# Kernel tuning notes

Hardware: AMD Instinct MI355X
Metric: run time of the kernel (lower is better)

The kernel has to match this reference:

```python
import jax, jax.numpy as jnp
import numpy as np

HEADS = 8


def _gat(X, A, Wq, Wk, Wv, Wo, units):
    B, N, _ = X.shape
    # QKV projections -> [B, H, N, units]
    Q = (X @ Wq).reshape(B, N, HEADS, units).transpose(0, 2, 1, 3)
    K = (X @ Wk).reshape(B, N, HEADS, units).transpose(0, 2, 1, 3)
    V = (X @ Wv).reshape(B, N, HEADS, units).transpose(0, 2, 1, 3)
    scores = jnp.einsum('bhnd,bhmd->bhnm', Q, K) / jnp.sqrt(jnp.float32(units))
    # source adds A * -1e9 (masks where A == 1)
    scores = scores + A[:, None, :, :] * (-1e9)
    w = jax.nn.softmax(scores, axis=-1)  # dropout off at inference
    ctx = jnp.einsum('bhnm,bhmd->bhnd', w, V)
    ctx = ctx.transpose(0, 2, 1, 3).reshape(B, N, HEADS * units)
    return ctx @ Wo


def setup_inputs() -> dict:
    key = jax.random.key(0)
    ks = jax.random.split(key, 16)
    B, N, F = 8, 1024, 64
    u1, u2 = 128, 64
    g = lambda k, s: (jax.random.normal(k, s, dtype=jnp.float32)
                      * np.sqrt(2.0 / (s[0] + s[-1])).astype(np.float32))
    X = jax.random.normal(ks[0], (B, N, F), dtype=jnp.float32)
    A = jax.random.bernoulli(ks[1], 0.5, (B, N, N)).astype(jnp.float32)
    return {
        'X': X, 'A': A,
        'Wq1': g(ks[2], (F, u1 * HEADS)), 'Wk1': g(ks[3], (F, u1 * HEADS)),
        'Wv1': g(ks[4], (F, u1 * HEADS)), 'Wo1': g(ks[5], (u1 * HEADS, u1)),
        'Wq2': g(ks[6], (u1, u2 * HEADS)), 'Wk2': g(ks[7], (u1, u2 * HEADS)),
        'Wv2': g(ks[8], (u1, u2 * HEADS)), 'Wo2': g(ks[9], (u2 * HEADS, u2)),
        'W1': g(ks[10], (u2, 32)), 'b1': jnp.zeros((32,), jnp.float32),
        'W2': g(ks[11], (32, 16)), 'b2': jnp.zeros((16,), jnp.float32),
        'W3': g(ks[12], (16, 1)), 'b3': jnp.zeros((1,), jnp.float32),
    }


def reference(X, A, Wq1, Wk1, Wv1, Wo1, Wq2, Wk2, Wv2, Wo2,
              W1, b1, W2, b2, W3, b3):
    h = _gat(X, A, Wq1, Wk1, Wv1, Wo1, 128)   # [B, N, 128]
    h = _gat(h, A, Wq2, Wk2, Wv2, Wo2, 64)    # [B, N, 64]
    h = jnp.mean(h, axis=1)                   # [B, 64]
    h = jax.nn.relu(h @ W1 + b1)
    h = jax.nn.relu(h @ W2 + b2)
    return h @ W3 + b3                        # [B, 1]
```

## Files before the change

### kernel.cpp

```cpp
#include <hip/hip_runtime.h>
#include <hip/hip_bf16.h>
#include <math.h>

#define NB 8
#define NN 1024
#define NH 8

typedef __attribute__((ext_vector_type(8))) short bf16x8;
typedef __attribute__((ext_vector_type(4))) float f32x4;
typedef unsigned int u32;
typedef unsigned short u16;

__device__ __forceinline__ u16 f2bf(float f) {
    union { float f; u32 u; } v; v.f = f;
    const u32 u = v.u;
    return (u16)((u + 0x7fffu + ((u >> 16) & 1u)) >> 16);
}

__device__ __forceinline__ u32 cvt_pk_bf16(float lo, float hi) {
    u32 r;
    asm("v_cvt_pk_bf16_f32 %0, %1, %2" : "=v"(r) : "v"(lo), "v"(hi));
    return r;
}

__global__ __launch_bounds__(256) void mask_bits(const float* __restrict__ A,
                                                 u32* __restrict__ bits) {
    const int row = blockIdx.x;
    const int tid = threadIdx.x;
    const int lane = tid & 63;
    const float* __restrict__ ar = A + (size_t)row * NN;
#pragma unroll
    for (int it = 0; it < 4; ++it) {
        const int i = it * 256 + tid;
        const unsigned long long bal = __ballot(ar[i] != 0.0f);
        const int w0 = (it * 256 + (tid & ~63)) >> 5;
        if (lane == 0)  bits[(size_t)row * 32 + w0]     = (u32)bal;
        if (lane == 32) bits[(size_t)row * 32 + w0 + 1] = (u32)(bal >> 32);
    }
}

__global__ __launch_bounds__(256)
void cvt_bf16(const float* __restrict__ in, u16* __restrict__ out) {
    const int i = blockIdx.x * 256 + threadIdx.x;
    const float4 a = ((const float4*)in)[2 * i];
    const float4 b = ((const float4*)in)[2 * i + 1];
    u16 t[8] = {f2bf(a.x), f2bf(a.y), f2bf(a.z), f2bf(a.w),
                f2bf(b.x), f2bf(b.y), f2bf(b.z), f2bf(b.w)};
    ((uint4*)out)[i] = *(uint4*)t;
}

template <int KIN, int HD>
__global__ __launch_bounds__(256)
void cvt_qkvT(const float* __restrict__ Wq, const float* __restrict__ Wk,
              const float* __restrict__ Wv, u16* __restrict__ WT) {
    const int idx = blockIdx.x * 256 + threadIdx.x;
    const int c  = idx / (KIN / 8);
    const int f0 = (idx % (KIN / 8)) * 8;
    const float* __restrict__ W = (c < HD) ? Wq : (c < 2 * HD) ? Wk : Wv;
    const int cc = c % HD;
    u16 tmp[8];
#pragma unroll
    for (int j = 0; j < 8; ++j)
        tmp[j] = f2bf(W[(size_t)(f0 + j) * HD + cc]);
    *(uint4*)&WT[(size_t)c * KIN + f0] = *(uint4*)tmp;
}

template <int CIN, int COUT>
__global__ __launch_bounds__(256)
void cvt_woT(const float* __restrict__ Wo, u16* __restrict__ WoT) {
    const int idx = blockIdx.x * 256 + threadIdx.x;
    const int n  = idx / (CIN / 8);
    const int k0 = (idx % (CIN / 8)) * 8;
    u16 tmp[8];
#pragma unroll
    for (int j = 0; j < 8; ++j)
        tmp[j] = f2bf(Wo[(size_t)(k0 + j) * COUT + n]);
    *(uint4*)&WoT[(size_t)n * CIN + k0] = *(uint4*)tmp;
}

template <int KIN, int HD, int D>
__global__ __launch_bounds__(256)
void proj_mfma(const u16* __restrict__ Xb,
               const u16* __restrict__ WT,
               u16* __restrict__ Qb,
               u16* __restrict__ Kb,
               u16* __restrict__ VT,
               const float qscale) {
    constexpr int NKT = KIN / 32;
    constexpr int NTW = (3 * HD / 16) / 4;

    const int tid  = threadIdx.x;
    const int w    = tid >> 6;
    const int lane = tid & 63;
    const int g    = lane >> 4;
    const int q16  = lane & 15;
    const int r0   = blockIdx.x * 16;
    const int b    = r0 >> 10;
    const int n0   = r0 & 1023;
    const int ch   = n0 >> 5;
    const int grp  = (n0 >> 4) & 1;

    bf16x8 af[NKT];
#pragma unroll
    for (int t = 0; t < NKT; ++t)
        af[t] = *(const bf16x8*)&Xb[(size_t)(r0 + q16) * KIN + t * 32 + g * 8];

#pragma unroll 1
    for (int i = 0; i < NTW; ++i) {
        const int nt = w + 4 * i;
        const int c0 = nt * 16;
        f32x4 acc = (f32x4)0.f;
#pragma unroll
        for (int t = 0; t < NKT; ++t) {
            const bf16x8 wf = *(const bf16x8*)&WT[(size_t)(c0 + q16) * KIN + t * 32 + g * 8];
            acc = __builtin_amdgcn_mfma_f32_16x16x32_bf16(af[t], wf, acc, 0, 0, 0);
        }

        const int wcl = c0 / HD;
        const int cc  = c0 % HD;
        const int h   = cc / D;
        const int d0  = cc % D;
        const int bh  = b * NH + h;

        if (wcl == 2) {
            u16 tmp[4];
#pragma unroll
            for (int r = 0; r < 4; ++r) tmp[r] = f2bf(acc[r]);
            *(uint2*)&VT[(((size_t)bh * 32 + ch) * D + d0 + q16) * 32
                         + 8 * g + 4 * grp] = *(uint2*)tmp;
        } else {
            u16* __restrict__ O = wcl ? Kb : Qb;
            const float sc = wcl ? 1.0f : qscale;
#pragma unroll
            for (int r = 0; r < 4; ++r)
                O[((size_t)bh * NN + n0 + 4 * g + r) * D + d0 + q16] = f2bf(acc[r] * sc);
        }
    }
}

template <int D>
__global__ __launch_bounds__(256, 2)
void attn_v12(const u16* __restrict__ Qb,
              const u16* __restrict__ Kb,
              const u16* __restrict__ VT,
              const u32* __restrict__ bits,
              u16* __restrict__ Ob) {
    constexpr int ND4 = D / 32;
    constexpr int NDT = D / 16;
    constexpr int KROWB = 2 * D;
    constexpr int KBYTES = 64 * KROWB;
    constexpr int KU = (D == 128) ? 4 : 2;

    const int tid  = threadIdx.x;
    const int w    = tid >> 6;
    const int lane = tid & 63;
    const int g    = lane >> 4;
    const int q16  = lane & 15;

    const int xcd    = blockIdx.x & 7;
    const int within = blockIdx.x >> 3;
    const int bh     = xcd * 8 + (within >> 3);
    const int b      = bh >> 3, h = bh & 7;
    const int q0     = ((within & 7) * 4 + w) * 32;

    const u16* __restrict__ qbase = Qb + (size_t)bh * NN * D;
    const u16* __restrict__ kbase = Kb + (size_t)bh * NN * D;
    const u16* __restrict__ vbase = VT + (size_t)bh * 32 * D * 32;
    const u32* __restrict__ brow0 = bits + ((size_t)b * NN + q0 + q16) * 32;
    const u32* __restrict__ brow1 = brow0 + 16 * 32;

    __shared__ alignas(16) char KsB[2][KBYTES];

    const int kRow = tid >> 2;
    const int kU0  = (tid & 3) * KU;

    bf16x8 qf[2][ND4];
#pragma unroll
    for (int qs = 0; qs < 2; ++qs)
#pragma unroll
        for (int f = 0; f < ND4; ++f)
            qf[qs][f] = *(const bf16x8*)
                &qbase[(size_t)(q0 + qs * 16 + q16) * D + f * 32 + g * 8];

    f32x4 acc[2][NDT];
    f32x4 accL[2];
#pragma unroll
    for (int qs = 0; qs < 2; ++qs) {
        accL[qs] = (f32x4)0.f;
#pragma unroll
        for (int dt = 0; dt < NDT; ++dt) acc[qs][dt] = (f32x4)0.f;
    }

    const short oneb = (short)0x3F80;
    const bf16x8 ones = {oneb, oneb, oneb, oneb, oneb, oneb, oneb, oneb};

    uint4 skr[KU];
    auto stage_load = [&](int ch) {
        const u16* src = kbase + (size_t)(ch * 64 + kRow) * D + kU0 * 8;
#pragma unroll
        for (int i = 0; i < KU; ++i) skr[i] = *(const uint4*)(src + i * 8);
    };
    auto stage_write = [&](int buf) {
        char* kr = KsB[buf] + kRow * KROWB;
#pragma unroll
        for (int i = 0; i < KU; ++i)
            *(uint4*)(kr + (((kU0 + i) ^ (kRow & 7)) * 16)) = skr[i];
    };

    stage_load(0);
    stage_write(0);
    stage_load(1);
    __syncthreads();

#pragma unroll 1
    for (int ch = 0; ch < 16; ++ch) {
        const int cur = ch & 1;
        if (ch + 1 < 16) stage_write(cur ^ 1);
        if (ch + 2 < 16) stage_load(ch + 2);

        bf16x8 vf[2][NDT];
#pragma unroll
        for (int kg = 0; kg < 2; ++kg)
#pragma unroll
            for (int dt = 0; dt < NDT; ++dt)
                vf[kg][dt] = *(const bf16x8*)
                    &vbase[((size_t)(ch * 2 + kg) * D + dt * 16 + q16) * 32 + 8 * g];

        const uint2 bwA = *(const uint2*)(brow0 + ch * 2);
        const uint2 bwB = *(const uint2*)(brow1 + ch * 2);

        f32x4 s[2][4];
#pragma unroll
        for (int qs = 0; qs < 2; ++qs)
#pragma unroll
            for (int kb = 0; kb < 4; ++kb) s[qs][kb] = (f32x4)0.f;

        __builtin_amdgcn_s_setprio(1);
#pragma unroll
        for (int kb = 0; kb < 4; ++kb) {
            bf16x8 kf[ND4];
#pragma unroll
            for (int f = 0; f < ND4; ++f)
                kf[f] = *(const bf16x8*)
                    (KsB[cur] + (kb * 16 + q16) * KROWB + (((f * 4 + g) ^ (q16 & 7)) * 16));
#pragma unroll
            for (int f = 0; f < ND4; ++f) {
                s[0][kb] = __builtin_amdgcn_mfma_f32_16x16x32_bf16(kf[f], qf[0][f], s[0][kb], 0, 0, 0);
                s[1][kb] = __builtin_amdgcn_mfma_f32_16x16x32_bf16(kf[f], qf[1][f], s[1][kb], 0, 0, 0);
            }
        }
        __builtin_amdgcn_s_setprio(0);

        union { u32 u[4]; bf16x8 v; } pa[2][2];
#pragma unroll
        for (int qs = 0; qs < 2; ++qs) {
            const u32 w0 = qs ? bwB.x : bwA.x;
            const u32 w1 = qs ? bwB.y : bwA.y;
#pragma unroll
            for (int kb = 0; kb < 4; ++kb) {
                const u32 sh = ((kb >> 1) ? w1 : w0) >> (g * 4 + (kb & 1) * 16);
                float p[4];
#pragma unroll
                for (int r = 0; r < 4; ++r) {
                    const float e = exp2f(s[qs][kb][r]);
                    p[r] = ((sh >> r) & 1u) ? 0.f : e;
                }
                pa[qs][kb >> 1].u[(kb & 1) * 2 + 0] = cvt_pk_bf16(p[0], p[1]);
                pa[qs][kb >> 1].u[(kb & 1) * 2 + 1] = cvt_pk_bf16(p[2], p[3]);
            }
        }

        __builtin_amdgcn_s_setprio(1);
#pragma unroll
        for (int kg = 0; kg < 2; ++kg) {
            accL[0] = __builtin_amdgcn_mfma_f32_16x16x32_bf16(pa[0][kg].v, ones, accL[0], 0, 0, 0);
            accL[1] = __builtin_amdgcn_mfma_f32_16x16x32_bf16(pa[1][kg].v, ones, accL[1], 0, 0, 0);
#pragma unroll
            for (int dt = 0; dt < NDT; ++dt) {
                acc[0][dt] = __builtin_amdgcn_mfma_f32_16x16x32_bf16(pa[0][kg].v, vf[kg][dt], acc[0][dt], 0, 0, 0);
                acc[1][dt] = __builtin_amdgcn_mfma_f32_16x16x32_bf16(pa[1][kg].v, vf[kg][dt], acc[1][dt], 0, 0, 0);
            }
        }
        __builtin_amdgcn_s_setprio(0);

        __syncthreads();
    }

#pragma unroll
    for (int qs = 0; qs < 2; ++qs) {
        float ivr[4];
#pragma unroll
        for (int r = 0; r < 4; ++r) ivr[r] = 1.0f / accL[qs][r];
#pragma unroll
        for (int dt = 0; dt < NDT; ++dt)
#pragma unroll
            for (int r = 0; r < 4; ++r) {
                const int q = q0 + qs * 16 + g * 4 + r;
                Ob[(((size_t)b * NN + q) * NH + h) * D + dt * 16 + q16] =
                    f2bf(acc[qs][dt][r] * ivr[r]);
            }
    }
}

template <int CIN, int COUT, bool BF16OUT>
__global__ __launch_bounds__(256)
void wo_mfma(const u16* __restrict__ ctxb,
             const u16* __restrict__ WoT,
             void* __restrict__ Hout) {
    constexpr int NTW = COUT / 64;
    const int tid  = threadIdx.x;
    const int w    = tid >> 6;
    const int lane = tid & 63;
    const int g    = lane >> 4;
    const int q16  = lane & 15;
    const int r0   = blockIdx.x * 16;

    f32x4 acc[NTW];
#pragma unroll
    for (int nt = 0; nt < NTW; ++nt) acc[nt] = (f32x4)0.f;

    const u16* __restrict__ arow = ctxb + (size_t)(r0 + q16) * CIN + g * 8;

#pragma unroll 4
    for (int k0 = 0; k0 < CIN; k0 += 32) {
        const bf16x8 af = *(const bf16x8*)(arow + k0);
#pragma unroll
        for (int nt = 0; nt < NTW; ++nt) {
            const int n = (w * NTW + nt) * 16 + q16;
            const bf16x8 wf = *(const bf16x8*)&WoT[(size_t)n * CIN + k0 + g * 8];
            acc[nt] = __builtin_amdgcn_mfma_f32_16x16x32_bf16(af, wf, acc[nt], 0, 0, 0);
        }
    }

#pragma unroll
    for (int nt = 0; nt < NTW; ++nt)
#pragma unroll
        for (int r = 0; r < 4; ++r) {
            const size_t off = (size_t)(r0 + 4 * g + r) * COUT + (w * NTW + nt) * 16 + q16;
            if constexpr (BF16OUT) ((u16*)Hout)[off] = f2bf(acc[nt][r]);
            else                   ((float*)Hout)[off] = acc[nt][r];
        }
}

__global__ __launch_bounds__(256)
void pool_partial(const float* __restrict__ H2, float* __restrict__ partial) {
    const int b  = blockIdx.x >> 5;
    const int ch = blockIdx.x & 31;
    const int tid = threadIdx.x;
    const int o = tid & 63;
    const int g = tid >> 6;

    __shared__ float red[4][64];
    float acc = 0.f;
#pragma unroll
    for (int i = 0; i < 8; ++i) {
        const int n = ch * 32 + g * 8 + i;
        acc += H2[((size_t)b * NN + n) * 64 + o];
    }
    red[g][o] = acc;
    __syncthreads();
    if (g == 0)
        partial[((size_t)b * 32 + ch) * 64 + o] =
            (red[0][o] + red[1][o]) + (red[2][o] + red[3][o]);
}

__global__ __launch_bounds__(256)
void pool_mlp2(const float* __restrict__ partial,
               const float* __restrict__ W1, const float* __restrict__ b1,
               const float* __restrict__ W2, const float* __restrict__ b2,
               const float* __restrict__ W3, const float* __restrict__ b3,
               float* __restrict__ out) {
    const int b = blockIdx.x;
    const int tid = threadIdx.x;
    const int o = tid & 63;
    const int g = tid >> 6;
    __shared__ float red[4][64];
    __shared__ float mean[64];
    __shared__ float h1[32];
    __shared__ float h2[16];

    float acc = 0.f;
#pragma unroll
    for (int c = 0; c < 8; ++c)
        acc += partial[((size_t)b * 32 + g * 8 + c) * 64 + o];
    red[g][o] = acc;
    __syncthreads();
    if (g == 0)
        mean[o] = ((red[0][o] + red[1][o]) + (red[2][o] + red[3][o])) * (1.0f / 1024.0f);
    __syncthreads();

    if (tid < 32) {
        float a = b1[tid];
#pragma unroll
        for (int f = 0; f < 64; ++f) a = fmaf(mean[f], W1[f * 32 + tid], a);
        h1[tid] = fmaxf(a, 0.f);
    }
    __syncthreads();
    if (tid < 16) {
        float a = b2[tid];
#pragma unroll
        for (int f = 0; f < 32; ++f) a = fmaf(h1[f], W2[f * 16 + tid], a);
        h2[tid] = fmaxf(a, 0.f);
    }
    __syncthreads();
    if (tid == 0) {
        float a = b3[0];
#pragma unroll
        for (int f = 0; f < 16; ++f) a = fmaf(h2[f], W3[f], a);
        out[b] = a;
    }
}

extern "C" void kernel_launch(void* const* d_in, const int* in_sizes, int n_in,
                              void* d_out, int out_size, void* d_ws, size_t ws_size,
                              hipStream_t stream) {
    const float* X   = (const float*)d_in[0];
    const float* A   = (const float*)d_in[1];
    const float* Wq1 = (const float*)d_in[2];
    const float* Wk1 = (const float*)d_in[3];
    const float* Wv1 = (const float*)d_in[4];
    const float* Wo1 = (const float*)d_in[5];
    const float* Wq2 = (const float*)d_in[6];
    const float* Wk2 = (const float*)d_in[7];
    const float* Wv2 = (const float*)d_in[8];
    const float* Wo2 = (const float*)d_in[9];
    const float* W1  = (const float*)d_in[10];
    const float* b1  = (const float*)d_in[11];
    const float* W2  = (const float*)d_in[12];
    const float* b2  = (const float*)d_in[13];
    const float* W3  = (const float*)d_in[14];
    const float* b3  = (const float*)d_in[15];
    float* out = (float*)d_out;

    u32* bits   = (u32*)d_ws;
    u16* base   = (u16*)(bits + 262144);
    u16* Qb1    = base;  base += 8388608;
    u16* Kb1    = base;  base += 8388608;
    u16* VT1    = base;  base += 8388608;
    u16* ctx1b  = base;  base += 8388608;
    u16* WoT1   = base;  base += 131072;
    u16* Qb2    = base;  base += 4194304;
    u16* Kb2    = base;  base += 4194304;
    u16* VT2    = base;  base += 4194304;
    u16* ctx2b  = base;  base += 4194304;
    u16* WoT2   = base;  base += 32768;
    u16* Xb     = base;  base += 524288;
    u16* WqkvT1 = base;  base += 196608;
    u16* WqkvT2 = base;  base += 196608;
    u16* H1b    = base;  base += 1048576;
    float* H2   = (float*)base;
    float* partial = H2 + 524288;

    const int ROWS = NB * NN;
    const float LOG2E = 1.4426950408889634f;

    mask_bits<<<ROWS, 256, 0, stream>>>(A, bits);
    cvt_bf16<<<ROWS * 64 / 8 / 256, 256, 0, stream>>>(X, Xb);
    cvt_qkvT<64, 1024><<<3072 * 64 / 8 / 256, 256, 0, stream>>>(Wq1, Wk1, Wv1, WqkvT1);
    cvt_qkvT<128, 512><<<1536 * 128 / 8 / 256, 256, 0, stream>>>(Wq2, Wk2, Wv2, WqkvT2);
    cvt_woT<1024, 128><<<128 * 1024 / 8 / 256, 256, 0, stream>>>(Wo1, WoT1);
    cvt_woT<512, 64><<<64 * 512 / 8 / 256, 256, 0, stream>>>(Wo2, WoT2);

    proj_mfma<64, 1024, 128><<<ROWS / 16, 256, 0, stream>>>(
        Xb, WqkvT1, Qb1, Kb1, VT1, 0.08838834764831845f * LOG2E);
    attn_v12<128><<<512, 256, 0, stream>>>(Qb1, Kb1, VT1, bits, ctx1b);
    wo_mfma<1024, 128, true><<<ROWS / 16, 256, 0, stream>>>(ctx1b, WoT1, H1b);

    proj_mfma<128, 512, 64><<<ROWS / 16, 256, 0, stream>>>(
        H1b, WqkvT2, Qb2, Kb2, VT2, 0.125f * LOG2E);
    attn_v12<64><<<512, 256, 0, stream>>>(Qb2, Kb2, VT2, bits, ctx2b);
    wo_mfma<512, 64, false><<<ROWS / 16, 256, 0, stream>>>(ctx2b, WoT2, H2);

    pool_partial<<<256, 256, 0, stream>>>(H2, partial);
    pool_mlp2<<<NB, 256, 0, stream>>>(partial, W1, b1, W2, b2, W3, b3, out);
}
```

Before: 252.0 us.

## Stage V tiles through double-buffered LDS and parametrize KV block size

The attention kernel now loads V chunks cooperatively into a padded, double-buffered shared-memory tile alongside K. Previously every wave read V fragments directly from global memory, so the four waves of a block each fetched the same data. The KV chunk size becomes a template parameter, 64 for the first layer and 128 for the second, which halves the loop trips and barriers in layer two. The cost is more LDS per block, which may affect occupancy at 2 blocks per CU, plus extra LDS traffic and register pressure.

Result: slower. 269.0 us (+6.7%).

```diff
diff --git a/kernel.cpp b/kernel.cpp
--- a/kernel.cpp
+++ b/kernel.cpp
@@ -138,18 +138,24 @@
     }
 }
 
-template <int D>
+template <int D, int KVBLK>
 __global__ __launch_bounds__(256, 2)
-void attn_v12(const u16* __restrict__ Qb,
+void attn_v13(const u16* __restrict__ Qb,
               const u16* __restrict__ Kb,
               const u16* __restrict__ VT,
               const u32* __restrict__ bits,
               u16* __restrict__ Ob) {
     constexpr int ND4 = D / 32;
     constexpr int NDT = D / 16;
+    constexpr int NCH = NN / KVBLK;
+    constexpr int NKB = KVBLK / 16;
+    constexpr int NKG = KVBLK / 32;
     constexpr int KROWB = 2 * D;
-    constexpr int KBYTES = 64 * KROWB;
-    constexpr int KU = (D == 128) ? 4 : 2;
+    constexpr int KBYTES = KVBLK * KROWB;
+    constexpr int VROWB = 2 * KVBLK + 16;
+    constexpr int VBYTES = D * VROWB;
+    constexpr int KTPR = KROWB / 64;
+    constexpr bool VPRE = (NKG <= 2);
 
     const int tid  = threadIdx.x;
     const int w    = tid >> 6;
@@ -170,9 +176,12 @@
     const u32* __restrict__ brow1 = brow0 + 16 * 32;
 
     __shared__ alignas(16) char KsB[2][KBYTES];
-
-    const int kRow = tid >> 2;
-    const int kU0  = (tid & 3) * KU;
+    __shared__ alignas(16) char VsB[2][VBYTES];
+
+    const int kRow = tid / KTPR;
+    const int kU0  = (tid % KTPR) * 4;
+    const int vD   = tid / NKG;
+    const int vSeg = tid % NKG;
 
     bf16x8 qf[2][ND4];
 #pragma unroll
@@ -194,17 +203,23 @@
     const short oneb = (short)0x3F80;
     const bf16x8 ones = {oneb, oneb, oneb, oneb, oneb, oneb, oneb, oneb};
 
-    uint4 skr[KU];
+    uint4 skr[4], svr[4];
     auto stage_load = [&](int ch) {
-        const u16* src = kbase + (size_t)(ch * 64 + kRow) * D + kU0 * 8;
-#pragma unroll
-        for (int i = 0; i < KU; ++i) skr[i] = *(const uint4*)(src + i * 8);
+        const u16* ksrc = kbase + (size_t)(ch * KVBLK + kRow) * D + kU0 * 8;
+#pragma unroll
+        for (int i = 0; i < 4; ++i) skr[i] = *(const uint4*)(ksrc + i * 8);
+        const u16* vsrc = vbase + ((size_t)(ch * NKG + vSeg) * D + vD) * 32;
+#pragma unroll
+        for (int i = 0; i < 4; ++i) svr[i] = *(const uint4*)(vsrc + i * 8);
     };
     auto stage_write = [&](int buf) {
         char* kr = KsB[buf] + kRow * KROWB;
 #pragma unroll
-        for (int i = 0; i < KU; ++i)
+        for (int i = 0; i < 4; ++i)
             *(uint4*)(kr + (((kU0 + i) ^ (kRow & 7)) * 16)) = skr[i];
+        char* vr = VsB[buf] + vD * VROWB + vSeg * 64;
+#pragma unroll
+        for (int i = 0; i < 4; ++i) *(uint4*)(vr + i * 16) = svr[i];
     };
 
     stage_load(0);
@@ -213,31 +228,27 @@
     __syncthreads();
 
 #pragma unroll 1
-    for (int ch = 0; ch < 16; ++ch) {
+    for (int ch = 0; ch < NCH; ++ch) {
         const int cur = ch & 1;
-        if (ch + 1 < 16) stage_write(cur ^ 1);
-        if (ch + 2 < 16) stage_load(ch + 2);
-
-        bf16x8 vf[2][NDT];
-#pragma unroll
-        for (int kg = 0; kg < 2; ++kg)
-#pragma unroll
-            for (int dt = 0; dt < NDT; ++dt)
-                vf[kg][dt] = *(const bf16x8*)
-                    &vbase[((size_t)(ch * 2 + kg) * D + dt * 16 + q16) * 32 + 8 * g];
-
-        const uint2 bwA = *(const uint2*)(brow0 + ch * 2);
-        const uint2 bwB = *(const uint2*)(brow1 + ch * 2);
-
-        f32x4 s[2][4];
+        if (ch + 1 < NCH) stage_write(cur ^ 1);
+        if (ch + 2 < NCH) stage_load(ch + 2);
+
+        u32 bw0[NKG], bw1[NKG];
+#pragma unroll
+        for (int i = 0; i < NKG; ++i) {
+            bw0[i] = brow0[ch * NKG + i];
+            bw1[i] = brow1[ch * NKG + i];
+        }
+
+        f32x4 s[2][NKB];
 #pragma unroll
         for (int qs = 0; qs < 2; ++qs)
 #pragma unroll
-            for (int kb = 0; kb < 4; ++kb) s[qs][kb] = (f32x4)0.f;
+            for (int kb = 0; kb < NKB; ++kb) s[qs][kb] = (f32x4)0.f;
 
         __builtin_amdgcn_s_setprio(1);
 #pragma unroll
-        for (int kb = 0; kb < 4; ++kb) {
+        for (int kb = 0; kb < NKB; ++kb) {
             bf16x8 kf[ND4];
 #pragma unroll
             for (int f = 0; f < ND4; ++f)
@@ -251,14 +262,23 @@
         }
         __builtin_amdgcn_s_setprio(0);
 
-        union { u32 u[4]; bf16x8 v; } pa[2][2];
+        bf16x8 vfp[VPRE ? 2 : 1][NDT];
+        if constexpr (VPRE) {
+#pragma unroll
+            for (int kg = 0; kg < 2; ++kg)
+#pragma unroll
+                for (int dt = 0; dt < NDT; ++dt)
+                    vfp[kg][dt] = *(const bf16x8*)
+                        (VsB[cur] + (dt * 16 + q16) * VROWB + kg * 64 + g * 16);
+        }
+
+        union { u32 u[4]; bf16x8 v; } pa[2][NKG];
 #pragma unroll
         for (int qs = 0; qs < 2; ++qs) {
-            const u32 w0 = qs ? bwB.x : bwA.x;
-            const u32 w1 = qs ? bwB.y : bwA.y;
-#pragma unroll
-            for (int kb = 0; kb < 4; ++kb) {
-                const u32 sh = ((kb >> 1) ? w1 : w0) >> (g * 4 + (kb & 1) * 16);
+#pragma unroll
+            for (int kb = 0; kb < NKB; ++kb) {
+                const u32 bwv = qs ? bw1[kb >> 1] : bw0[kb >> 1];
+                const u32 sh = bwv >> (g * 4 + (kb & 1) * 16);
                 float p[4];
 #pragma unroll
                 for (int r = 0; r < 4; ++r) {
@@ -272,13 +292,17 @@
 
         __builtin_amdgcn_s_setprio(1);
 #pragma unroll
-        for (int kg = 0; kg < 2; ++kg) {
+        for (int kg = 0; kg < NKG; ++kg) {
             accL[0] = __builtin_amdgcn_mfma_f32_16x16x32_bf16(pa[0][kg].v, ones, accL[0], 0, 0, 0);
             accL[1] = __builtin_amdgcn_mfma_f32_16x16x32_bf16(pa[1][kg].v, ones, accL[1], 0, 0, 0);
 #pragma unroll
             for (int dt = 0; dt < NDT; ++dt) {
-                acc[0][dt] = __builtin_amdgcn_mfma_f32_16x16x32_bf16(pa[0][kg].v, vf[kg][dt], acc[0][dt], 0, 0, 0);
-                acc[1][dt] = __builtin_amdgcn_mfma_f32_16x16x32_bf16(pa[1][kg].v, vf[kg][dt], acc[1][dt], 0, 0, 0);
+                bf16x8 vf;
+                if constexpr (VPRE) vf = vfp[kg][dt];
+                else vf = *(const bf16x8*)
+                    (VsB[cur] + (dt * 16 + q16) * VROWB + kg * 64 + g * 16);
+                acc[0][dt] = __builtin_amdgcn_mfma_f32_16x16x32_bf16(pa[0][kg].v, vf, acc[0][dt], 0, 0, 0);
+                acc[1][dt] = __builtin_amdgcn_mfma_f32_16x16x32_bf16(pa[1][kg].v, vf, acc[1][dt], 0, 0, 0);
             }
         }
         __builtin_amdgcn_s_setprio(0);
@@ -463,12 +487,12 @@
 
     proj_mfma<64, 1024, 128><<<ROWS / 16, 256, 0, stream>>>(
         Xb, WqkvT1, Qb1, Kb1, VT1, 0.08838834764831845f * LOG2E);
-    attn_v12<128><<<512, 256, 0, stream>>>(Qb1, Kb1, VT1, bits, ctx1b);
+    attn_v13<128, 64><<<512, 256, 0, stream>>>(Qb1, Kb1, VT1, bits, ctx1b);
     wo_mfma<1024, 128, true><<<ROWS / 16, 256, 0, stream>>>(ctx1b, WoT1, H1b);
 
     proj_mfma<128, 512, 64><<<ROWS / 16, 256, 0, stream>>>(
         H1b, WqkvT2, Qb2, Kb2, VT2, 0.125f * LOG2E);
-    attn_v12<64><<<512, 256, 0, stream>>>(Qb2, Kb2, VT2, bits, ctx2b);
+    attn_v13<64, 128><<<512, 256, 0, stream>>>(Qb2, Kb2, VT2, bits, ctx2b);
     wo_mfma<512, 64, false><<<ROWS / 16, 256, 0, stream>>>(ctx2b, WoT2, H2);
 
     pool_partial<<<256, 256, 0, stream>>>(H2, partial);
```
